# Optimization experiments

Measured on AMD Instinct MI355X. Metric: run time of the kernel, lower is better.

## Reference

```python
import jax, jax.numpy as jnp
import numpy as np

ACTION_DIM = 7
CHUNK_SIZE = 4
INPUT_DIM = ACTION_DIM * CHUNK_SIZE  # 28
HIDDEN = 128
LATENT = 64
NUM_CODES = 512
COMMITMENT_COST = 0.25
BATCH = 262144


def setup_inputs() -> dict:
    key = jax.random.key(0)
    ks = jax.random.split(key, 10)

    def lin_init(k, fan_in, fan_out):
        # torch nn.Linear default: U(-1/sqrt(fan_in), 1/sqrt(fan_in)) for W and b
        bound = 1.0 / np.sqrt(fan_in)
        kw, kb = jax.random.split(k)
        W = jax.random.uniform(kw, (fan_in, fan_out), jnp.float32, -bound, bound)
        b = jax.random.uniform(kb, (fan_out,), jnp.float32, -bound, bound)
        return W, b

    x = jax.random.normal(ks[0], (BATCH, INPUT_DIM), jnp.float32)
    enc_w1, enc_b1 = lin_init(ks[1], INPUT_DIM, HIDDEN)
    enc_w2, enc_b2 = lin_init(ks[2], HIDDEN, LATENT)
    codebook = jax.random.uniform(
        ks[3], (NUM_CODES, LATENT), jnp.float32, -1.0 / NUM_CODES, 1.0 / NUM_CODES
    )
    dec_w1, dec_b1 = lin_init(ks[4], LATENT, HIDDEN)
    dec_w2, dec_b2 = lin_init(ks[5], HIDDEN, INPUT_DIM)
    return {
        "x": x,
        "enc_w1": enc_w1, "enc_b1": enc_b1,
        "enc_w2": enc_w2, "enc_b2": enc_b2,
        "codebook": codebook,
        "dec_w1": dec_w1, "dec_b1": dec_b1,
        "dec_w2": dec_w2, "dec_b2": dec_b2,
    }


def reference(x, enc_w1, enc_b1, enc_w2, enc_b2, codebook,
              dec_w1, dec_b1, dec_w2, dec_b2):
    sg = jax.lax.stop_gradient
    # Encoder: Linear -> ReLU -> Linear
    h = jax.nn.relu(x @ enc_w1 + enc_b1)          # (B, 128)
    z = h @ enc_w2 + enc_b2                       # (B, 64)
    # Nearest-code lookup: ||z||^2 + ||e||^2 - 2 z.e
    z2 = jnp.sum(z * z, axis=1, keepdims=True)    # (B, 1)
    e2 = jnp.sum(codebook * codebook, axis=1)     # (C,)
    ze = z @ codebook.T                           # (B, C) dominant intermediate
    distances = z2 + e2 - 2.0 * ze
    indices = jnp.argmin(distances, axis=1)       # (B,)
    quantized = codebook[indices]                 # (B, 64) gather
    # VQ losses
    codebook_loss = jnp.mean((sg(z) - quantized) ** 2)
    commitment_loss = jnp.mean((z - sg(quantized)) ** 2)
    vq_loss = codebook_loss + COMMITMENT_COST * commitment_loss
    # Straight-through estimator
    z_q = z + sg(quantized - z)
    # Decoder
    hd = jax.nn.relu(z_q @ dec_w1 + dec_b1)       # (B, 128)
    recon = hd @ dec_w2 + dec_b2                  # (B, 28)
    recon_loss = jnp.mean((recon - x) ** 2)
    return recon, recon_loss, vq_loss
```

## Files before the change

### kernel.cpp

```cpp
#include <hip/hip_runtime.h>

#define BATCH   262144
#define IN_DIM  28
#define HID     128
#define LAT     64
#define NCODES  512
#define NBLK    256
#define WVS     16
#define NWAVE   (NBLK * WVS)

#define S1 40
#define S2 136
#define SC 72
#define O_LW1 0
#define O_LW2 5120
#define O_LCB 13824
#define O_LD1 50688
#define O_LD2 59904
#define BLOB_SHORTS 64256
#define BLOB_F32    864
#define BLOB_BYTES  (BLOB_SHORTS * 2 + BLOB_F32 * 4)
#define LDS_BYTES   BLOB_BYTES

#define E2_BASE   BLOB_SHORTS
#define B1_BASE   (BLOB_SHORTS + 4096)
#define B2_BASE   (B1_BASE + 128)
#define DB1_BASE  (B2_BASE + 64)
#define DB2_BASE  (DB1_BASE + 128)
#define PREP_END  (DB2_BASE + 32)

typedef short v4s __attribute__((ext_vector_type(4)));
typedef short v8s __attribute__((ext_vector_type(8)));
typedef float v4f __attribute__((ext_vector_type(4)));

union u2v4 { unsigned u[2]; v4s s; };

__device__ __forceinline__ unsigned short f2bf(float f) {
  unsigned u = __float_as_uint(f);
  u += 0x7fffu + ((u >> 16) & 1u);
  return (unsigned short)(u >> 16);
}
__device__ __forceinline__ unsigned pk(float hi, float lo) {
  return __builtin_amdgcn_perm(__float_as_uint(hi), __float_as_uint(lo), 0x07060302u);
}
__device__ __forceinline__ float xf0(unsigned u) { return __uint_as_float(u << 16); }
__device__ __forceinline__ float xf1(unsigned u) { return __uint_as_float(u & 0xFFFF0000u); }

__device__ __forceinline__ v4f mfma16(v4s a, v4s b, v4f c) {
  return __builtin_amdgcn_mfma_f32_16x16x16bf16_1k(a, b, c, 0, 0, 0);
}
__device__ __forceinline__ v4s lo4(v8s v) { return __builtin_shufflevector(v, v, 0, 1, 2, 3); }
__device__ __forceinline__ v4s hi4(v8s v) { return __builtin_shufflevector(v, v, 4, 5, 6, 7); }

__device__ __forceinline__ v4s rlpk(v4f h) {
  u2v4 c;
  c.u[0] = pk(fmaxf(h[1], 0.f), fmaxf(h[0], 0.f));
  c.u[1] = pk(fmaxf(h[3], 0.f), fmaxf(h[2], 0.f));
  return c.s;
}
__device__ __forceinline__ v4s zpk(v4f z) {
  u2v4 c; c.u[0] = pk(z[1], z[0]); c.u[1] = pk(z[3], z[2]); return c.s;
}
__device__ __forceinline__ v4s mkv(unsigned a, unsigned b) {
  u2v4 c; c.u[0] = a; c.u[1] = b; return c.s;
}
__device__ __forceinline__ float kpack(float d, unsigned code) {
  return __uint_as_float((__float_as_uint(d) & 0xFFFFFE00u) | code);
}

__global__ __launch_bounds__(256) void vq_prep(
    const float* __restrict__ ew1, const float* __restrict__ eb1,
    const float* __restrict__ ew2, const float* __restrict__ eb2,
    const float* __restrict__ cb,  const float* __restrict__ dw1,
    const float* __restrict__ db1, const float* __restrict__ dw2,
    const float* __restrict__ db2,
    unsigned short* __restrict__ blob) {
  int i = blockIdx.x * 256 + threadIdx.x;
  float* fb = (float*)(blob + BLOB_SHORTS);
  if (i < O_LW2) {
    int row = i / S1, s = i % S1;
    unsigned short v = 0;
    if (s < 32) {
      int q = s >> 3, r2 = s & 7, j = r2 >> 2, e = r2 & 3;
      int k = j * 16 + q * 4 + e;
      if (k < IN_DIM) v = f2bf(ew1[k * HID + row]);
    }
    blob[i] = v;
  } else if (i < O_LCB) {
    int j2 = i - O_LW2; int row = j2 / S2, s = j2 % S2;
    unsigned short v = 0;
    if (s < 128) {
      int q = s >> 5, r2 = s & 31, j = r2 >> 2, e = r2 & 3;
      int k = j * 16 + q * 4 + e;
      v = f2bf(ew2[k * LAT + row]);
    }
    blob[i] = v;
  } else if (i < O_LD1) {
    int j2 = i - O_LCB; int row = j2 / SC, s = j2 % SC;
    unsigned short v = 0;
    if (s < 64) {
      int q = s >> 4, r2 = s & 15, j = r2 >> 2, e = r2 & 3;
      int k = j * 16 + q * 4 + e;
      v = f2bf(-2.0f * cb[row * LAT + k]);
    }
    blob[i] = v;
  } else if (i < O_LD2) {
    int j2 = i - O_LD1; int row = j2 / SC, s = j2 % SC;
    unsigned short v = 0;
    if (s < 64) {
      int q = s >> 4, r2 = s & 15, j = r2 >> 2, e = r2 & 3;
      int k = j * 16 + q * 4 + e;
      v = f2bf(-0.5f * dw1[k * HID + row]);
    }
    blob[i] = v;
  } else if (i < BLOB_SHORTS) {
    int j2 = i - O_LD2; int row = j2 / S2, s = j2 % S2;
    unsigned short v = 0;
    if (s < 128 && row < IN_DIM) {
      int q = s >> 5, r2 = s & 31, j = r2 >> 2, e = r2 & 3;
      int k = j * 16 + q * 4 + e;
      v = f2bf(dw2[k * IN_DIM + row]);
    }
    blob[i] = v;
  } else if (i < B1_BASE) {
    int j = i - E2_BASE;
    int c = j >> 3, l = j & 7;
    const float* p = cb + c * LAT + l * 8;
    float4 a = *(const float4*)p;
    float4 b = *(const float4*)(p + 4);
    float s = a.x * a.x + a.y * a.y + a.z * a.z + a.w * a.w
            + b.x * b.x + b.y * b.y + b.z * b.z + b.w * b.w;
    s += __shfl_xor(s, 1, 64);
    s += __shfl_xor(s, 2, 64);
    s += __shfl_xor(s, 4, 64);
    if (l == 0) fb[c] = s;
  } else if (i < B2_BASE) {
    fb[512 + (i - B1_BASE)] = eb1[i - B1_BASE];
  } else if (i < DB1_BASE) {
    fb[640 + (i - B2_BASE)] = eb2[i - B2_BASE];
  } else if (i < DB2_BASE) {
    fb[704 + (i - DB1_BASE)] = db1[i - DB1_BASE];
  } else if (i < PREP_END) {
    int k = i - DB2_BASE;
    fb[832 + k] = (k < IN_DIM) ? db2[k] : 0.f;
  }
}

__device__ __forceinline__ void s12_pair(
    const unsigned short* __restrict__ L, const float* __restrict__ LF,
    int lm, int quad,
    v4s bxa_lo, v4s bxa_hi, v4s bxb_lo, v4s bxb_hi,
    v4s& zfa0, v4s& zfa1, v4s& zfa2, v4s& zfa3,
    v4s& zfb0, v4s& zfb1, v4s& zfb2, v4s& zfb3,
    float& z2a, float& z2b) {
  const int fw1 = O_LW1 + lm * S1 + quad * 8;
  const int fw2 = O_LW2 + lm * S2 + quad * 32;
  v4f za[4], zb[4];
#pragma unroll
  for (int nt = 0; nt < 4; ++nt) {
    v4f s = *(const v4f*)&LF[640 + nt * 16 + quad * 4];
    za[nt] = s; zb[nt] = s;
  }
#pragma unroll 1
  for (int jp = 0; jp < 4; ++jp) {
    v4s hA0, hA1, hB0, hB1;
    {
      v8s w = *(const v8s*)&L[fw1 + (2 * jp) * (16 * S1)];
      v4f sd = *(const v4f*)&LF[512 + (2 * jp) * 16 + quad * 4];
      v4f h = mfma16(lo4(w), bxa_lo, sd);
      h = mfma16(hi4(w), bxa_hi, h);
      hA0 = rlpk(h);
      h = mfma16(lo4(w), bxb_lo, sd);
      h = mfma16(hi4(w), bxb_hi, h);
      hB0 = rlpk(h);
    }
    {
      v8s w = *(const v8s*)&L[fw1 + (2 * jp + 1) * (16 * S1)];
      v4f sd = *(const v4f*)&LF[512 + (2 * jp + 1) * 16 + quad * 4];
      v4f h = mfma16(lo4(w), bxa_lo, sd);
      h = mfma16(hi4(w), bxa_hi, h);
      hA1 = rlpk(h);
      h = mfma16(lo4(w), bxb_lo, sd);
      h = mfma16(hi4(w), bxb_hi, h);
      hB1 = rlpk(h);
    }
#pragma unroll
    for (int nt = 0; nt < 4; ++nt) {
      v8s w2 = *(const v8s*)&L[fw2 + nt * (16 * S2) + jp * 8];
      za[nt] = mfma16(lo4(w2), hA0, za[nt]);
      za[nt] = mfma16(hi4(w2), hA1, za[nt]);
      zb[nt] = mfma16(lo4(w2), hB0, zb[nt]);
      zb[nt] = mfma16(hi4(w2), hB1, zb[nt]);
    }
  }
  z2a = za[0][0] * za[0][0] + za[0][1] * za[0][1] + za[0][2] * za[0][2] + za[0][3] * za[0][3]
      + za[1][0] * za[1][0] + za[1][1] * za[1][1] + za[1][2] * za[1][2] + za[1][3] * za[1][3]
      + za[2][0] * za[2][0] + za[2][1] * za[2][1] + za[2][2] * za[2][2] + za[2][3] * za[2][3]
      + za[3][0] * za[3][0] + za[3][1] * za[3][1] + za[3][2] * za[3][2] + za[3][3] * za[3][3];
  z2b = zb[0][0] * zb[0][0] + zb[0][1] * zb[0][1] + zb[0][2] * zb[0][2] + zb[0][3] * zb[0][3]
      + zb[1][0] * zb[1][0] + zb[1][1] * zb[1][1] + zb[1][2] * zb[1][2] + zb[1][3] * zb[1][3]
      + zb[2][0] * zb[2][0] + zb[2][1] * zb[2][1] + zb[2][2] * zb[2][2] + zb[2][3] * zb[2][3]
      + zb[3][0] * zb[3][0] + zb[3][1] * zb[3][1] + zb[3][2] * zb[3][2] + zb[3][3] * zb[3][3];
  zfa0 = zpk(za[0]); zfa1 = zpk(za[1]); zfa2 = zpk(za[2]); zfa3 = zpk(za[3]);
  zfb0 = zpk(zb[0]); zfb1 = zpk(zb[1]); zfb2 = zpk(zb[2]); zfb3 = zpk(zb[3]);
}

__device__ __forceinline__ void s56_pair(
    const unsigned short* __restrict__ L, const float* __restrict__ LF,
    int lm, int quad, int codeA, int codeB,
    unsigned xa0, unsigned xa1, unsigned xa2, unsigned xa3,
    unsigned xb0, unsigned xb1, unsigned xb2, unsigned xb3,
    float* __restrict__ orowA, float* __restrict__ orowB, float& racc) {
  const int fd1 = O_LD1 + lm * SC + quad * 16;
  const int fd2 = O_LD2 + lm * S2 + quad * 32;
  const int gA = O_LCB + codeA * SC + quad * 16;
  const int gB = O_LCB + codeB * SC + quad * 16;
  v8s qa0 = *(const v8s*)&L[gA];
  v8s qa1 = *(const v8s*)&L[gA + 8];
  v8s qb0 = *(const v8s*)&L[gB];
  v8s qb1 = *(const v8s*)&L[gB + 8];
  v4f a6a[2], a6b[2];
#pragma unroll
  for (int nt = 0; nt < 2; ++nt) {
    v4f s = *(const v4f*)&LF[832 + nt * 16 + quad * 4];
    a6a[nt] = s; a6b[nt] = s;
  }
#pragma unroll 1
  for (int jp = 0; jp < 4; ++jp) {
    v4s hA0, hA1, hB0, hB1;
#pragma unroll
    for (int jj = 0; jj < 2; ++jj) {
      int j = 2 * jp + jj;
      v8s d0 = *(const v8s*)&L[fd1 + j * (16 * SC)];
      v8s d1 = *(const v8s*)&L[fd1 + j * (16 * SC) + 8];
      v4f sd = *(const v4f*)&LF[704 + j * 16 + quad * 4];
      v4f h = mfma16(lo4(d0), lo4(qa0), sd);
      h = mfma16(hi4(d0), hi4(qa0), h);
      h = mfma16(lo4(d1), lo4(qa1), h);
      h = mfma16(hi4(d1), hi4(qa1), h);
      v4s ha = rlpk(h);
      h = mfma16(lo4(d0), lo4(qb0), sd);
      h = mfma16(hi4(d0), hi4(qb0), h);
      h = mfma16(lo4(d1), lo4(qb1), h);
      h = mfma16(hi4(d1), hi4(qb1), h);
      v4s hb = rlpk(h);
      if (jj == 0) { hA0 = ha; hB0 = hb; } else { hA1 = ha; hB1 = hb; }
    }
#pragma unroll
    for (int nt = 0; nt < 2; ++nt) {
      v8s w6 = *(const v8s*)&L[fd2 + nt * (16 * S2) + jp * 8];
      a6a[nt] = mfma16(lo4(w6), hA0, a6a[nt]);
      a6a[nt] = mfma16(hi4(w6), hA1, a6a[nt]);
      a6b[nt] = mfma16(lo4(w6), hB0, a6b[nt]);
      a6b[nt] = mfma16(hi4(w6), hB1, a6b[nt]);
    }
  }
  *(float4*)(orowA + quad * 4) = (float4){a6a[0][0], a6a[0][1], a6a[0][2], a6a[0][3]};
  *(float4*)(orowB + quad * 4) = (float4){a6b[0][0], a6b[0][1], a6b[0][2], a6b[0][3]};
  if (quad < 3) {
    *(float4*)(orowA + 16 + quad * 4) = (float4){a6a[1][0], a6a[1][1], a6a[1][2], a6a[1][3]};
    *(float4*)(orowB + 16 + quad * 4) = (float4){a6b[1][0], a6b[1][1], a6b[1][2], a6b[1][3]};
  }
  float d;
  d = a6a[0][0] - xf0(xa0); racc += d * d;
  d = a6a[0][1] - xf1(xa0); racc += d * d;
  d = a6a[0][2] - xf0(xa1); racc += d * d;
  d = a6a[0][3] - xf1(xa1); racc += d * d;
  d = a6a[1][0] - xf0(xa2); racc += d * d;
  d = a6a[1][1] - xf1(xa2); racc += d * d;
  d = a6a[1][2] - xf0(xa3); racc += d * d;
  d = a6a[1][3] - xf1(xa3); racc += d * d;
  d = a6b[0][0] - xf0(xb0); racc += d * d;
  d = a6b[0][1] - xf1(xb0); racc += d * d;
  d = a6b[0][2] - xf0(xb1); racc += d * d;
  d = a6b[0][3] - xf1(xb1); racc += d * d;
  d = a6b[1][0] - xf0(xb2); racc += d * d;
  d = a6b[1][1] - xf1(xb2); racc += d * d;
  d = a6b[1][2] - xf0(xb3); racc += d * d;
  d = a6b[1][3] - xf1(xb3); racc += d * d;
}

__global__ __attribute__((amdgpu_flat_work_group_size(1024, 1024)))
__attribute__((amdgpu_waves_per_eu(4, 4)))
void vq_main(
    const float* __restrict__ x,
    const unsigned short* __restrict__ blob,
    float* __restrict__ out, float* __restrict__ partials) {

  extern __shared__ __align__(16) char smem[];
  const unsigned short* L = (const unsigned short*)smem;
  const float*         LF = (const float*)(smem + BLOB_SHORTS * 2);

  const int tid  = threadIdx.x;
  const int wave = tid >> 6;
  const int lane = tid & 63;
  const int quad = lane >> 4;
  const int lm   = lane & 15;

  {
    const float4* src = (const float4*)blob;
    float4* dst = (float4*)smem;
#pragma unroll
    for (int it = 0; it < 9; ++it) {
      int idx = it * 1024 + tid;
      if (idx < BLOB_BYTES / 16) dst[idx] = src[idx];
    }
  }
  __syncthreads();

  const int rbase = blockIdx.x * 1024 + wave * 64;
  float racc = 0.f, vqacc = 0.f;

#pragma unroll 1
  for (int sw = 0; sw < 2; ++sw) {
    const int r0 = rbase + sw * 32;

    unsigned xa0, xa1, xa2, xa3, xb0, xb1, xb2, xb3;
    {
      const float* xpa = x + (size_t)(r0 + lm) * IN_DIM;
      const float* xpb = x + (size_t)(r0 + 16 + lm) * IN_DIM;
      float4 t = *(const float4*)(xpa + quad * 4);
      xa0 = pk(t.y, t.x); xa1 = pk(t.w, t.z);
      t = (quad < 3) ? *(const float4*)(xpa + 16 + quad * 4) : (float4){0.f, 0.f, 0.f, 0.f};
      xa2 = pk(t.y, t.x); xa3 = pk(t.w, t.z);
      t = *(const float4*)(xpb + quad * 4);
      xb0 = pk(t.y, t.x); xb1 = pk(t.w, t.z);
      t = (quad < 3) ? *(const float4*)(xpb + 16 + quad * 4) : (float4){0.f, 0.f, 0.f, 0.f};
      xb2 = pk(t.y, t.x); xb3 = pk(t.w, t.z);
    }

    v4s zfa0, zfa1, zfa2, zfa3, zfb0, zfb1, zfb2, zfb3;
    float z2a, z2b;
    s12_pair(L, LF, lm, quad,
             mkv(xa0, xa1), mkv(xa2, xa3), mkv(xb0, xb1), mkv(xb2, xb3),
             zfa0, zfa1, zfa2, zfa3, zfb0, zfb1, zfb2, zfb3, z2a, z2b);
    __builtin_amdgcn_sched_barrier(0);

    const int fcb = O_LCB + lm * SC + quad * 16;
    float bkA = __uint_as_float(0x7f7fffffu);
    float bkB = bkA;
#pragma unroll 2
    for (int ct = 0; ct < 32; ++ct) {
      v8s c0 = *(const v8s*)&L[fcb + ct * (16 * SC)];
      v8s c1 = *(const v8s*)&L[fcb + ct * (16 * SC) + 8];
      v4f sd = *(const v4f*)&LF[ct * 16 + quad * 4];
      v4f dA = mfma16(lo4(c0), zfa0, sd);
      dA = mfma16(hi4(c0), zfa1, dA);
      dA = mfma16(lo4(c1), zfa2, dA);
      dA = mfma16(hi4(c1), zfa3, dA);
      v4f dB = mfma16(lo4(c0), zfb0, sd);
      dB = mfma16(hi4(c0), zfb1, dB);
      dB = mfma16(lo4(c1), zfb2, dB);
      dB = mfma16(hi4(c1), zfb3, dB);
      unsigned cbase = (unsigned)(ct * 16 + quad * 4);
      bkA = fminf(bkA, fminf(fminf(kpack(dA[0], cbase), kpack(dA[1], cbase + 1)),
                             fminf(kpack(dA[2], cbase + 2), kpack(dA[3], cbase + 3))));
      bkB = fminf(bkB, fminf(fminf(kpack(dB[0], cbase), kpack(dB[1], cbase + 1)),
                             fminf(kpack(dB[2], cbase + 2), kpack(dB[3], cbase + 3))));
    }

#pragma unroll
    for (int off = 16; off < 64; off <<= 1) {
      bkA = fminf(bkA, __shfl_xor(bkA, off, 64));
      bkB = fminf(bkB, __shfl_xor(bkB, off, 64));
      z2a += __shfl_xor(z2a, off, 64);
      z2b += __shfl_xor(z2b, off, 64);
    }
    unsigned ka = __float_as_uint(bkA), kb = __float_as_uint(bkB);
    int codeA = (int)(ka & 511u), codeB = (int)(kb & 511u);
    if (quad == 0)
      vqacc += z2a + __uint_as_float(ka & 0xFFFFFE00u)
             + z2b + __uint_as_float(kb & 0xFFFFFE00u);
    __builtin_amdgcn_sched_barrier(0);

    s56_pair(L, LF, lm, quad, codeA, codeB,
             xa0, xa1, xa2, xa3, xb0, xb1, xb2, xb3,
             out + (size_t)(r0 + lm) * IN_DIM,
             out + (size_t)(r0 + 16 + lm) * IN_DIM, racc);
    __builtin_amdgcn_sched_barrier(0);
  }

#pragma unroll
  for (int off = 1; off < 64; off <<= 1) {
    racc  += __shfl_xor(racc, off, 64);
    vqacc += __shfl_xor(vqacc, off, 64);
  }
  if (lane == 0) {
    size_t w = (size_t)blockIdx.x * WVS + wave;
    partials[w * 2]     = racc;
    partials[w * 2 + 1] = vqacc;
  }
}

__global__ __launch_bounds__(256) void vq_fin(const float* __restrict__ partials,
                                              float* __restrict__ out) {
  float r = 0.f, v = 0.f;
  for (int i = threadIdx.x; i < NWAVE; i += 256) {
    r += partials[2 * i];
    v += partials[2 * i + 1];
  }
#pragma unroll
  for (int off = 1; off < 64; off <<= 1) {
    r += __shfl_xor(r, off, 64);
    v += __shfl_xor(v, off, 64);
  }
  __shared__ float s[4][2];
  int w = threadIdx.x >> 6;
  if ((threadIdx.x & 63) == 0) { s[w][0] = r; s[w][1] = v; }
  __syncthreads();
  if (threadIdx.x == 0) {
    float R = s[0][0] + s[1][0] + s[2][0] + s[3][0];
    float V = s[0][1] + s[1][1] + s[2][1] + s[3][1];
    out[7340032] = R * (1.0f / 7340032.0f);
    out[7340033] = V * (1.25f / 16777216.0f);
  }
}

extern "C" void kernel_launch(void* const* d_in, const int* in_sizes, int n_in,
                              void* d_out, int out_size, void* d_ws, size_t ws_size,
                              hipStream_t stream) {
  const float* x   = (const float*)d_in[0];
  const float* ew1 = (const float*)d_in[1];
  const float* eb1 = (const float*)d_in[2];
  const float* ew2 = (const float*)d_in[3];
  const float* eb2 = (const float*)d_in[4];
  const float* cb  = (const float*)d_in[5];
  const float* dw1 = (const float*)d_in[6];
  const float* db1 = (const float*)d_in[7];
  const float* dw2 = (const float*)d_in[8];
  const float* db2 = (const float*)d_in[9];

  char* ws = (char*)d_ws;
  unsigned short* blob = (unsigned short*)(ws + 0);
  float* partials = (float*)(ws + 132096);

  float* out = (float*)d_out;

  (void)hipFuncSetAttribute((const void*)vq_main,
                            hipFuncAttributeMaxDynamicSharedMemorySize, LDS_BYTES);

  vq_prep<<<(PREP_END + 255) / 256, 256, 0, stream>>>(
      ew1, eb1, ew2, eb2, cb, dw1, db1, dw2, db2, blob);
  vq_main<<<NBLK, 1024, LDS_BYTES, stream>>>(x, blob, out, partials);
  vq_fin<<<1, 256, 0, stream>>>(partials, out);
}
```

Measured before the change: 134.5 us.

## Fuse weight prep and final reduction into main kernel, fold encoder bias into MFMA

Removes the separate prep and finalize kernels. Each block now converts and swizzles the weights from global memory straight into LDS, and the final loss reduction runs in the last block to finish, tracked by an atomic counter. The first-layer encoder bias is folded into the weight matrix as an extra input column fed by a constant 1 in the padded x lane, so the bias load from LDS goes away. This trades two kernel launches and a global blob round-trip for redundant per-block conversion work, which is 256 blocks each reading all weights, plus a memset and atomic synchronisation.

```diff
diff --git a/kernel.cpp b/kernel.cpp
--- a/kernel.cpp
+++ b/kernel.cpp
@@ -7,7 +7,6 @@
 #define NCODES  512
 #define NBLK    256
 #define WVS     16
-#define NWAVE   (NBLK * WVS)
 
 #define S1 40
 #define S2 136
@@ -18,16 +17,9 @@
 #define O_LD1 50688
 #define O_LD2 59904
 #define BLOB_SHORTS 64256
-#define BLOB_F32    864
+#define BLOB_F32    736
 #define BLOB_BYTES  (BLOB_SHORTS * 2 + BLOB_F32 * 4)
 #define LDS_BYTES   BLOB_BYTES
-
-#define E2_BASE   BLOB_SHORTS
-#define B1_BASE   (BLOB_SHORTS + 4096)
-#define B2_BASE   (B1_BASE + 128)
-#define DB1_BASE  (B2_BASE + 64)
-#define DB2_BASE  (DB1_BASE + 128)
-#define PREP_END  (DB2_BASE + 32)
 
 typedef short v4s __attribute__((ext_vector_type(4)));
 typedef short v8s __attribute__((ext_vector_type(8)));
@@ -67,83 +59,8 @@
 __device__ __forceinline__ float kpack(float d, unsigned code) {
   return __uint_as_float((__float_as_uint(d) & 0xFFFFFE00u) | code);
 }
-
-__global__ __launch_bounds__(256) void vq_prep(
-    const float* __restrict__ ew1, const float* __restrict__ eb1,
-    const float* __restrict__ ew2, const float* __restrict__ eb2,
-    const float* __restrict__ cb,  const float* __restrict__ dw1,
-    const float* __restrict__ db1, const float* __restrict__ dw2,
-    const float* __restrict__ db2,
-    unsigned short* __restrict__ blob) {
-  int i = blockIdx.x * 256 + threadIdx.x;
-  float* fb = (float*)(blob + BLOB_SHORTS);
-  if (i < O_LW2) {
-    int row = i / S1, s = i % S1;
-    unsigned short v = 0;
-    if (s < 32) {
-      int q = s >> 3, r2 = s & 7, j = r2 >> 2, e = r2 & 3;
-      int k = j * 16 + q * 4 + e;
-      if (k < IN_DIM) v = f2bf(ew1[k * HID + row]);
-    }
-    blob[i] = v;
-  } else if (i < O_LCB) {
-    int j2 = i - O_LW2; int row = j2 / S2, s = j2 % S2;
-    unsigned short v = 0;
-    if (s < 128) {
-      int q = s >> 5, r2 = s & 31, j = r2 >> 2, e = r2 & 3;
-      int k = j * 16 + q * 4 + e;
-      v = f2bf(ew2[k * LAT + row]);
-    }
-    blob[i] = v;
-  } else if (i < O_LD1) {
-    int j2 = i - O_LCB; int row = j2 / SC, s = j2 % SC;
-    unsigned short v = 0;
-    if (s < 64) {
-      int q = s >> 4, r2 = s & 15, j = r2 >> 2, e = r2 & 3;
-      int k = j * 16 + q * 4 + e;
-      v = f2bf(-2.0f * cb[row * LAT + k]);
-    }
-    blob[i] = v;
-  } else if (i < O_LD2) {
-    int j2 = i - O_LD1; int row = j2 / SC, s = j2 % SC;
-    unsigned short v = 0;
-    if (s < 64) {
-      int q = s >> 4, r2 = s & 15, j = r2 >> 2, e = r2 & 3;
-      int k = j * 16 + q * 4 + e;
-      v = f2bf(-0.5f * dw1[k * HID + row]);
-    }
-    blob[i] = v;
-  } else if (i < BLOB_SHORTS) {
-    int j2 = i - O_LD2; int row = j2 / S2, s = j2 % S2;
-    unsigned short v = 0;
-    if (s < 128 && row < IN_DIM) {
-      int q = s >> 5, r2 = s & 31, j = r2 >> 2, e = r2 & 3;
-      int k = j * 16 + q * 4 + e;
-      v = f2bf(dw2[k * IN_DIM + row]);
-    }
-    blob[i] = v;
-  } else if (i < B1_BASE) {
-    int j = i - E2_BASE;
-    int c = j >> 3, l = j & 7;
-    const float* p = cb + c * LAT + l * 8;
-    float4 a = *(const float4*)p;
-    float4 b = *(const float4*)(p + 4);
-    float s = a.x * a.x + a.y * a.y + a.z * a.z + a.w * a.w
-            + b.x * b.x + b.y * b.y + b.z * b.z + b.w * b.w;
-    s += __shfl_xor(s, 1, 64);
-    s += __shfl_xor(s, 2, 64);
-    s += __shfl_xor(s, 4, 64);
-    if (l == 0) fb[c] = s;
-  } else if (i < B2_BASE) {
-    fb[512 + (i - B1_BASE)] = eb1[i - B1_BASE];
-  } else if (i < DB1_BASE) {
-    fb[640 + (i - B2_BASE)] = eb2[i - B2_BASE];
-  } else if (i < DB2_BASE) {
-    fb[704 + (i - DB1_BASE)] = db1[i - DB1_BASE];
-  } else if (i < PREP_END) {
-    int k = i - DB2_BASE;
-    fb[832 + k] = (k < IN_DIM) ? db2[k] : 0.f;
-  }
+__device__ __forceinline__ int swz(int k, int Kq) {
+  return ((k >> 2) & 3) * Kq + (k >> 4) * 4 + (k & 3);
 }
 
 __device__ __forceinline__ void s12_pair(
@@ -158,7 +75,7 @@
   v4f za[4], zb[4];
 #pragma unroll
   for (int nt = 0; nt < 4; ++nt) {
-    v4f s = *(const v4f*)&LF[640 + nt * 16 + quad * 4];
+    v4f s = *(const v4f*)&LF[512 + nt * 16 + quad * 4];
     za[nt] = s; zb[nt] = s;
   }
 #pragma unroll 1
@@ -166,21 +83,21 @@
     v4s hA0, hA1, hB0, hB1;
     {
       v8s w = *(const v8s*)&L[fw1 + (2 * jp) * (16 * S1)];
-      v4f sd = *(const v4f*)&LF[512 + (2 * jp) * 16 + quad * 4];
-      v4f h = mfma16(lo4(w), bxa_lo, sd);
+      v4f zero = {0.f, 0.f, 0.f, 0.f};
+      v4f h = mfma16(lo4(w), bxa_lo, zero);
       h = mfma16(hi4(w), bxa_hi, h);
       hA0 = rlpk(h);
-      h = mfma16(lo4(w), bxb_lo, sd);
+      h = mfma16(lo4(w), bxb_lo, zero);
       h = mfma16(hi4(w), bxb_hi, h);
       hB0 = rlpk(h);
     }
     {
       v8s w = *(const v8s*)&L[fw1 + (2 * jp + 1) * (16 * S1)];
-      v4f sd = *(const v4f*)&LF[512 + (2 * jp + 1) * 16 + quad * 4];
-      v4f h = mfma16(lo4(w), bxa_lo, sd);
+      v4f zero = {0.f, 0.f, 0.f, 0.f};
+      v4f h = mfma16(lo4(w), bxa_lo, zero);
       h = mfma16(hi4(w), bxa_hi, h);
       hA1 = rlpk(h);
-      h = mfma16(lo4(w), bxb_lo, sd);
+      h = mfma16(lo4(w), bxb_lo, zero);
       h = mfma16(hi4(w), bxb_hi, h);
       hB1 = rlpk(h);
     }
@@ -222,7 +139,7 @@
   v4f a6a[2], a6b[2];
 #pragma unroll
   for (int nt = 0; nt < 2; ++nt) {
-    v4f s = *(const v4f*)&LF[832 + nt * 16 + quad * 4];
+    v4f s = *(const v4f*)&LF[704 + nt * 16 + quad * 4];
     a6a[nt] = s; a6b[nt] = s;
   }
 #pragma unroll 1
@@ -233,7 +150,7 @@
       int j = 2 * jp + jj;
       v8s d0 = *(const v8s*)&L[fd1 + j * (16 * SC)];
       v8s d1 = *(const v8s*)&L[fd1 + j * (16 * SC) + 8];
-      v4f sd = *(const v4f*)&LF[704 + j * 16 + quad * 4];
+      v4f sd = *(const v4f*)&LF[576 + j * 16 + quad * 4];
       v4f h = mfma16(lo4(d0), lo4(qa0), sd);
       h = mfma16(hi4(d0), hi4(qa0), h);
       h = mfma16(lo4(d1), lo4(qa1), h);
@@ -266,30 +183,39 @@
   d = a6a[0][1] - xf1(xa0); racc += d * d;
   d = a6a[0][2] - xf0(xa1); racc += d * d;
   d = a6a[0][3] - xf1(xa1); racc += d * d;
-  d = a6a[1][0] - xf0(xa2); racc += d * d;
-  d = a6a[1][1] - xf1(xa2); racc += d * d;
-  d = a6a[1][2] - xf0(xa3); racc += d * d;
-  d = a6a[1][3] - xf1(xa3); racc += d * d;
   d = a6b[0][0] - xf0(xb0); racc += d * d;
   d = a6b[0][1] - xf1(xb0); racc += d * d;
   d = a6b[0][2] - xf0(xb1); racc += d * d;
   d = a6b[0][3] - xf1(xb1); racc += d * d;
-  d = a6b[1][0] - xf0(xb2); racc += d * d;
-  d = a6b[1][1] - xf1(xb2); racc += d * d;
-  d = a6b[1][2] - xf0(xb3); racc += d * d;
-  d = a6b[1][3] - xf1(xb3); racc += d * d;
+  if (quad < 3) {
+    d = a6a[1][0] - xf0(xa2); racc += d * d;
+    d = a6a[1][1] - xf1(xa2); racc += d * d;
+    d = a6a[1][2] - xf0(xa3); racc += d * d;
+    d = a6a[1][3] - xf1(xa3); racc += d * d;
+    d = a6b[1][0] - xf0(xb2); racc += d * d;
+    d = a6b[1][1] - xf1(xb2); racc += d * d;
+    d = a6b[1][2] - xf0(xb3); racc += d * d;
+    d = a6b[1][3] - xf1(xb3); racc += d * d;
+  }
 }
 
 __global__ __attribute__((amdgpu_flat_work_group_size(1024, 1024)))
 __attribute__((amdgpu_waves_per_eu(4, 4)))
 void vq_main(
     const float* __restrict__ x,
-    const unsigned short* __restrict__ blob,
-    float* __restrict__ out, float* __restrict__ partials) {
+    const float* __restrict__ ew1, const float* __restrict__ eb1,
+    const float* __restrict__ ew2, const float* __restrict__ eb2,
+    const float* __restrict__ cb,  const float* __restrict__ dw1,
+    const float* __restrict__ db1, const float* __restrict__ dw2,
+    const float* __restrict__ db2,
+    float* __restrict__ out, float* __restrict__ partials,
+    unsigned* __restrict__ counter) {
 
   extern __shared__ __align__(16) char smem[];
+  unsigned short* Lw = (unsigned short*)smem;
   const unsigned short* L = (const unsigned short*)smem;
-  const float*         LF = (const float*)(smem + BLOB_SHORTS * 2);
+  float* fbw = (float*)(smem + BLOB_SHORTS * 2);
+  const float* LF = (const float*)(smem + BLOB_SHORTS * 2);
 
   const int tid  = threadIdx.x;
   const int wave = tid >> 6;
@@ -298,13 +224,53 @@
   const int lm   = lane & 15;
 
   {
-    const float4* src = (const float4*)blob;
-    float4* dst = (float4*)smem;
-#pragma unroll
-    for (int it = 0; it < 9; ++it) {
+    float4* z4 = (float4*)smem;
+    float4 z = {0.f, 0.f, 0.f, 0.f};
+#pragma unroll
+    for (int it = 0; it < 8; ++it) {
       int idx = it * 1024 + tid;
-      if (idx < BLOB_BYTES / 16) dst[idx] = src[idx];
-    }
+      if (idx < BLOB_SHORTS / 8) z4[idx] = z;
+    }
+  }
+  __syncthreads();
+  {
+    for (int t = tid; t < IN_DIM * HID; t += 1024) {
+      int k = t >> 7, row = t & 127;
+      Lw[O_LW1 + row * S1 + swz(k, 8)] = f2bf(ew1[t]);
+    }
+    if (tid < HID)
+      Lw[O_LW1 + tid * S1 + 28] = f2bf(eb1[tid]);
+    for (int t = tid; t < HID * LAT; t += 1024) {
+      int k = t >> 6, row = t & 63;
+      Lw[O_LW2 + row * S2 + swz(k, 32)] = f2bf(ew2[t]);
+    }
+    for (int t = tid; t < NCODES * LAT; t += 1024) {
+      int c = t >> 6, d = t & 63;
+      Lw[O_LCB + c * SC + swz(d, 16)] = f2bf(-2.0f * cb[t]);
+    }
+    for (int t = tid; t < LAT * HID; t += 1024) {
+      int k = t >> 7, row = t & 127;
+      Lw[O_LD1 + row * SC + swz(k, 16)] = f2bf(-0.5f * dw1[t]);
+    }
+    for (int t = tid; t < HID * IN_DIM; t += 1024) {
+      int k = t / IN_DIM, n = t - k * IN_DIM;
+      Lw[O_LD2 + n * S2 + swz(k, 32)] = f2bf(dw2[t]);
+    }
+    for (int t = tid; t < NCODES * 8; t += 1024) {
+      int c = t >> 3, l = t & 7;
+      const float* p = cb + c * LAT + l * 8;
+      float4 a = *(const float4*)p;
+      float4 b = *(const float4*)(p + 4);
+      float s = a.x * a.x + a.y * a.y + a.z * a.z + a.w * a.w
+              + b.x * b.x + b.y * b.y + b.z * b.z + b.w * b.w;
+      s += __shfl_xor(s, 1, 64);
+      s += __shfl_xor(s, 2, 64);
+      s += __shfl_xor(s, 4, 64);
+      if (l == 0) fbw[c] = s;
+    }
+    if (tid < 64)  fbw[512 + tid] = eb2[tid];
+    if (tid < 128) fbw[576 + tid] = db1[tid];
+    if (tid < 32)  fbw[704 + tid] = (tid < IN_DIM) ? db2[tid] : 0.f;
   }
   __syncthreads();
 
@@ -321,11 +287,13 @@
       const float* xpb = x + (size_t)(r0 + 16 + lm) * IN_DIM;
       float4 t = *(const float4*)(xpa + quad * 4);
       xa0 = pk(t.y, t.x); xa1 = pk(t.w, t.z);
-      t = (quad < 3) ? *(const float4*)(xpa + 16 + quad * 4) : (float4){0.f, 0.f, 0.f, 0.f};
+      t = (quad < 3) ? *(const float4*)(xpa + 16 + quad * 4)
+                     : (float4){1.f, 0.f, 0.f, 0.f};
       xa2 = pk(t.y, t.x); xa3 = pk(t.w, t.z);
       t = *(const float4*)(xpb + quad * 4);
       xb0 = pk(t.y, t.x); xb1 = pk(t.w, t.z);
-      t = (quad < 3) ? *(const float4*)(xpb + 16 + quad * 4) : (float4){0.f, 0.f, 0.f, 0.f};
+      t = (quad < 3) ? *(const float4*)(xpb + 16 + quad * 4)
+                     : (float4){1.f, 0.f, 0.f, 0.f};
       xb2 = pk(t.y, t.x); xb3 = pk(t.w, t.z);
     }
 
@@ -385,34 +353,40 @@
     racc  += __shfl_xor(racc, off, 64);
     vqacc += __shfl_xor(vqacc, off, 64);
   }
-  if (lane == 0) {
-    size_t w = (size_t)blockIdx.x * WVS + wave;
-    partials[w * 2]     = racc;
-    partials[w * 2 + 1] = vqacc;
-  }
-}
-
-__global__ __launch_bounds__(256) void vq_fin(const float* __restrict__ partials,
-                                              float* __restrict__ out) {
-  float r = 0.f, v = 0.f;
-  for (int i = threadIdx.x; i < NWAVE; i += 256) {
-    r += partials[2 * i];
-    v += partials[2 * i + 1];
-  }
-#pragma unroll
-  for (int off = 1; off < 64; off <<= 1) {
-    r += __shfl_xor(r, off, 64);
-    v += __shfl_xor(v, off, 64);
-  }
-  __shared__ float s[4][2];
-  int w = threadIdx.x >> 6;
-  if ((threadIdx.x & 63) == 0) { s[w][0] = r; s[w][1] = v; }
   __syncthreads();
-  if (threadIdx.x == 0) {
-    float R = s[0][0] + s[1][0] + s[2][0] + s[3][0];
-    float V = s[0][1] + s[1][1] + s[2][1] + s[3][1];
-    out[7340032] = R * (1.0f / 7340032.0f);
-    out[7340033] = V * (1.25f / 16777216.0f);
+  float* sc = (float*)smem;
+  if (lane == 0) { sc[wave * 2] = racc; sc[wave * 2 + 1] = vqacc; }
+  __syncthreads();
+  int* flag = (int*)(smem + 256);
+  if (tid == 0) {
+    float R = 0.f, V = 0.f;
+#pragma unroll
+    for (int w = 0; w < WVS; ++w) { R += sc[2 * w]; V += sc[2 * w + 1]; }
+    partials[blockIdx.x * 2]     = R;
+    partials[blockIdx.x * 2 + 1] = V;
+    __threadfence();
+    unsigned t = atomicAdd(counter, 1u);
+    *flag = (t == NBLK - 1) ? 1 : 0;
+  }
+  __syncthreads();
+  if (*flag) {
+    __threadfence();
+    float r = 0.f, v = 0.f;
+    if (tid < NBLK) { r = partials[2 * tid]; v = partials[2 * tid + 1]; }
+#pragma unroll
+    for (int off = 1; off < 64; off <<= 1) {
+      r += __shfl_xor(r, off, 64);
+      v += __shfl_xor(v, off, 64);
+    }
+    if (lane == 0) { sc[64 + wave * 2] = r; sc[64 + wave * 2 + 1] = v; }
+    __syncthreads();
+    if (tid == 0) {
+      float R = 0.f, V = 0.f;
+#pragma unroll
+      for (int w = 0; w < 4; ++w) { R += sc[64 + 2 * w]; V += sc[64 + 2 * w + 1]; }
+      out[7340032] = R * (1.0f / 7340032.0f);
+      out[7340033] = V * (1.25f / 16777216.0f);
+    }
   }
 }
 
@@ -431,16 +405,15 @@
   const float* db2 = (const float*)d_in[9];
 
   char* ws = (char*)d_ws;
-  unsigned short* blob = (unsigned short*)(ws + 0);
-  float* partials = (float*)(ws + 132096);
+  float* partials = (float*)ws;
+  unsigned* counter = (unsigned*)(ws + 2048);
 
   float* out = (float*)d_out;
 
   (void)hipFuncSetAttribute((const void*)vq_main,
                             hipFuncAttributeMaxDynamicSharedMemorySize, LDS_BYTES);
 
-  vq_prep<<<(PREP_END + 255) / 256, 256, 0, stream>>>(
-      ew1, eb1, ew2, eb2, cb, dw1, db1, dw2, db2, blob);
-  vq_main<<<NBLK, 1024, LDS_BYTES, stream>>>(x, blob, out, partials);
-  vq_fin<<<1, 256, 0, stream>>>(partials, out);
-}
+  (void)hipMemsetAsync(counter, 0, 4, stream);
+  vq_main<<<NBLK, 1024, LDS_BYTES, stream>>>(
+      x, ew1, eb1, ew2, eb2, cb, dw1, db1, dw2, db2, out, partials, counter);
+}
```

After: 144.1 us. +7.2%, slower.
